# Optimization experiments

Hardware: AMD Instinct MI355X
Metric: run time of the kernel (lower is better)

The kernel has to match this reference:

```python
import jax, jax.numpy as jnp
import numpy as np

EPS = 1e-6
DIM = 2048
N_HEADS = 16
HEAD_DIM = DIM // N_HEADS  # 128
SEQ = 1040
CACHE = 8320
BATCH = 1


def rms_norm(x, g):
    # RMSNorm over the full model dim (WanRMSNorm)
    var = jnp.mean(jnp.square(x.astype(jnp.float32)), axis=-1, keepdims=True)
    return (x.astype(jnp.float32) * jax.lax.rsqrt(var + EPS)).astype(x.dtype) * g


def rope_apply(x, freqs):
    # x: [b, s, n, d]; freqs: [s, d//2] rotation angles (complex rotation on interleaved pairs)
    b, s, n, d = x.shape
    xr = x.reshape(b, s, n, d // 2, 2)
    xe, xo = xr[..., 0], xr[..., 1]
    cos = jnp.cos(freqs)[None, :, None, :]  # [1, s, 1, d//2]
    sin = jnp.sin(freqs)[None, :, None, :]
    out = jnp.stack([xe * cos - xo * sin, xe * sin + xo * cos], axis=-1)
    return out.reshape(b, s, n, d)


def sdpa(q, k, v):
    # q: [b, sq, n, d]; k, v: [b, skv, n, d]
    d = q.shape[-1]
    scale = 1.0 / jnp.sqrt(jnp.asarray(d, dtype=q.dtype))
    scores = jnp.einsum('bqnd,bknd->bnqk', q, k) * scale
    p = jax.nn.softmax(scores, axis=-1)
    return jnp.einsum('bnqk,bknd->bqnd', p, v)


def setup_inputs() -> dict:
    key = jax.random.key(0)
    ks = jax.random.split(key, 16)
    sc = 1.0 / np.sqrt(DIM)
    inp = {
        'x': jax.random.normal(ks[0], (BATCH, SEQ, DIM), dtype=jnp.float32),
        'seq_lens': jnp.full((BATCH,), SEQ, dtype=jnp.int32),
        'freqs': jax.random.uniform(ks[1], (SEQ, HEAD_DIM // 2), dtype=jnp.float32, maxval=2 * np.pi),
        'kv_cache_k': jax.random.normal(ks[2], (BATCH, CACHE, N_HEADS, HEAD_DIM), dtype=jnp.float32),
        'kv_cache_v': jax.random.normal(ks[3], (BATCH, CACHE, N_HEADS, HEAD_DIM), dtype=jnp.float32),
        'Wq': jax.random.normal(ks[4], (DIM, DIM), dtype=jnp.float32) * sc,
        'bq': jnp.zeros((DIM,), dtype=jnp.float32),
        'Wk': jax.random.normal(ks[5], (DIM, DIM), dtype=jnp.float32) * sc,
        'bk': jnp.zeros((DIM,), dtype=jnp.float32),
        'Wv': jax.random.normal(ks[6], (DIM, DIM), dtype=jnp.float32) * sc,
        'bv': jnp.zeros((DIM,), dtype=jnp.float32),
        'Wo': jax.random.normal(ks[7], (DIM, DIM), dtype=jnp.float32) * sc,
        'bo': jnp.zeros((DIM,), dtype=jnp.float32),
        'g_q': jnp.ones((DIM,), dtype=jnp.float32),
        'g_k': jnp.ones((DIM,), dtype=jnp.float32),
        'kv_start': 0,
        'kv_len': CACHE,
    }
    return inp


def reference(x, seq_lens, freqs, kv_cache_k, kv_cache_v, Wq, bq, Wk, bk, Wv, bv, Wo, bo, g_q, g_k, kv_start, kv_len):
    b, s, dim = x.shape
    d = 2 * freqs.shape[-1]
    n = dim // d
    q = rms_norm(x @ Wq + bq, g_q).reshape(b, s, n, d)
    k = rms_norm(x @ Wk + bk, g_k).reshape(b, s, n, d)
    v = (x @ Wv + bv).reshape(b, s, n, d)
    rq = rope_apply(q, freqs)
    rk = rope_apply(k, freqs)
    # kv_size[1] > 0 branch: concat cached KV slice with the new chunk
    k_full = jnp.concatenate([kv_cache_k[:, kv_start:kv_start + kv_len], rk], axis=1)
    v_full = jnp.concatenate([kv_cache_v[:, kv_start:kv_start + kv_len], v], axis=1)
    o = sdpa(rq, k_full, v_full)  # [b, s, n, d]
    return o.reshape(b, s, n * d) @ Wo + bo
```

## Files before the change

### kernel.cpp

```cpp
#include <hip/hip_runtime.h>

using bf16x8 = __attribute__((ext_vector_type(8))) short;
using f32x4  = __attribute__((ext_vector_type(4))) float;

#define DEV static __device__ __forceinline__

constexpr int SEQ    = 1040;
constexpr int MDIM   = 2048;
constexpr int NH     = 16;
constexpr int HD     = 128;
constexpr int NCACHE = 8320;
constexpr int LTOT   = NCACHE + SEQ;
constexpr int KROWS  = 9408;
constexpr int NQT2   = 9;

DEV float b2f(unsigned short u) {
  union { unsigned int i; float f; } z; z.i = ((unsigned int)u) << 16; return z.f;
}
DEV unsigned short f2b(float f) {
  union { float f; unsigned int i; } z; z.f = f;
  return (unsigned short)((z.i + 0x7fffu + ((z.i >> 16) & 1u)) >> 16);
}
DEV unsigned int cvtpk(float lo, float hi) {
  unsigned int r;
  asm("v_cvt_pk_bf16_f32 %0, %1, %2" : "=v"(r) : "v"(lo), "v"(hi));
  return r;
}
union U4S8 { uint4 u; short s[8]; };

__global__ __launch_bounds__(256) void convx_k(
    const float* __restrict__ x, unsigned short* __restrict__ xb, int n8) {
  int i = blockIdx.x * 256 + threadIdx.x;
  if (i < n8) {
    const float* p = x + (size_t)i * 8;
    f32x4 a = *(const f32x4*)p, b = *(const f32x4*)(p + 4);
    uint4 u = make_uint4(cvtpk(a[0], a[1]), cvtpk(a[2], a[3]),
                         cvtpk(b[0], b[1]), cvtpk(b[2], b[3]));
    *(uint4*)(xb + (size_t)i * 8) = u;
  }
}

__global__ __launch_bounds__(256) void convkv_k(
    const float* __restrict__ Kc, const float* __restrict__ Vc,
    unsigned short* __restrict__ Kb, unsigned short* __restrict__ Vb, int n8) {
  int i = blockIdx.x * 256 + threadIdx.x;
  const float* src = blockIdx.y ? Vc : Kc;
  unsigned short* dst = blockIdx.y ? Vb : Kb;
  if (i < n8) {
    const float* p = src + (size_t)i * 8;
    f32x4 a = *(const f32x4*)p, b = *(const f32x4*)(p + 4);
    uint4 u = make_uint4(cvtpk(a[0], a[1]), cvtpk(a[2], a[3]),
                         cvtpk(b[0], b[1]), cvtpk(b[2], b[3]));
    *(uint4*)(dst + (size_t)i * 8) = u;
  }
}

__global__ __launch_bounds__(256) void convt_k(
    const float* __restrict__ W0, const float* __restrict__ W1,
    const float* __restrict__ W2, const float* __restrict__ W3,
    unsigned short* __restrict__ T0, unsigned short* __restrict__ T1,
    unsigned short* __restrict__ T2, unsigned short* __restrict__ T3) {
  __shared__ short T[64][72];
  const int zz = blockIdx.z;
  const float* W = (zz == 0) ? W0 : (zz == 1) ? W1 : (zz == 2) ? W2 : W3;
  unsigned short* O = (zz == 0) ? T0 : (zz == 1) ? T1 : (zz == 2) ? T2 : T3;
  const int r0 = blockIdx.y * 64, c0 = blockIdx.x * 64;
  const int t = threadIdx.x;
  {
    int row = t >> 2, cq = t & 3;
    const float* p = W + (size_t)(r0 + row) * MDIM + c0 + cq * 16;
    f32x4 a = *(const f32x4*)(p);
    f32x4 b = *(const f32x4*)(p + 4);
    f32x4 c = *(const f32x4*)(p + 8);
    f32x4 d = *(const f32x4*)(p + 12);
    *(uint4*)&T[row][cq * 16] =
        make_uint4(cvtpk(a[0], a[1]), cvtpk(a[2], a[3]), cvtpk(b[0], b[1]), cvtpk(b[2], b[3]));
    *(uint4*)&T[row][cq * 16 + 8] =
        make_uint4(cvtpk(c[0], c[1]), cvtpk(c[2], c[3]), cvtpk(d[0], d[1]), cvtpk(d[2], d[3]));
  }
  __syncthreads();
  {
    int c = t >> 2, kq = t & 3;
    U4S8 v0, v1;
#pragma unroll
    for (int i = 0; i < 8; ++i) v0.s[i] = T[kq * 16 + i][c];
#pragma unroll
    for (int i = 0; i < 8; ++i) v1.s[i] = T[kq * 16 + 8 + i][c];
    unsigned short* op = O + (size_t)(c0 + c) * MDIM + r0 + kq * 16;
    *(uint4*)(op) = v0.u;
    *(uint4*)(op + 8) = v1.u;
  }
}

__global__ __launch_bounds__(256) void gemm_qkv_k(
    const unsigned short* __restrict__ xb,
    const unsigned short* __restrict__ Wtq, const unsigned short* __restrict__ Wtk,
    const unsigned short* __restrict__ Wtv,
    const float* __restrict__ bq, const float* __restrict__ bk, const float* __restrict__ bv,
    unsigned short* __restrict__ Qb, unsigned short* __restrict__ Kb, unsigned short* __restrict__ Vb) {
  __shared__ short As[64][72];
  __shared__ short Bs[128][72];
  const int tid = threadIdx.x;
  const int l = tid & 63, wv = tid >> 6;
  const int l16 = l & 15, kl = l >> 4;
  const int m0 = blockIdx.y * 64;
  const int n0g = blockIdx.x * 128;
  const int which = n0g >> 11;
  const int n0 = n0g & 2047;
  const unsigned short* Wt = (which == 0) ? Wtq : (which == 1) ? Wtk : Wtv;
  const float* bias = (which == 0) ? bq : (which == 1) ? bk : bv;
  const int wm = (wv >> 1) * 32, wn = (wv & 1) * 64;
  f32x4 acc[2][4] = {};
  for (int k0 = 0; k0 < MDIM; k0 += 64) {
    {
      int m = tid >> 2, kq = tid & 3;
      int row = m0 + m;
      uint4 v0 = make_uint4(0, 0, 0, 0), v1 = make_uint4(0, 0, 0, 0);
      if (row < SEQ) {
        const unsigned short* p = xb + (size_t)row * MDIM + k0 + kq * 16;
        v0 = *(const uint4*)p;
        v1 = *(const uint4*)(p + 8);
      }
      *(uint4*)&As[m][kq * 16] = v0;
      *(uint4*)&As[m][kq * 16 + 8] = v1;
    }
    {
      int n = tid >> 1, kq = tid & 1;
      const unsigned short* p = Wt + (size_t)(n0 + n) * MDIM + k0 + kq * 32;
      uint4 v0 = *(const uint4*)p, v1 = *(const uint4*)(p + 8);
      uint4 v2 = *(const uint4*)(p + 16), v3 = *(const uint4*)(p + 24);
      *(uint4*)&Bs[n][kq * 32] = v0;
      *(uint4*)&Bs[n][kq * 32 + 8] = v1;
      *(uint4*)&Bs[n][kq * 32 + 16] = v2;
      *(uint4*)&Bs[n][kq * 32 + 24] = v3;
    }
    __syncthreads();
#pragma unroll
    for (int kk = 0; kk < 2; ++kk) {
      bf16x8 aF[2], bF[4];
#pragma unroll
      for (int mi = 0; mi < 2; ++mi)
        aF[mi] = *(const bf16x8*)&As[wm + mi * 16 + l16][kk * 32 + kl * 8];
#pragma unroll
      for (int ni = 0; ni < 4; ++ni)
        bF[ni] = *(const bf16x8*)&Bs[wn + ni * 16 + l16][kk * 32 + kl * 8];
#pragma unroll
      for (int mi = 0; mi < 2; ++mi)
#pragma unroll
        for (int ni = 0; ni < 4; ++ni)
          acc[mi][ni] = __builtin_amdgcn_mfma_f32_16x16x32_bf16(
              aF[mi], bF[ni], acc[mi][ni], 0, 0, 0);
    }
    __syncthreads();
  }
#pragma unroll
  for (int ni = 0; ni < 4; ++ni) {
    const int col = n0 + wn + ni * 16 + l16;
    const float bb = bias[col];
#pragma unroll
    for (int mi = 0; mi < 2; ++mi) {
      const int rowb = m0 + wm + mi * 16 + kl * 4;
#pragma unroll
      for (int r = 0; r < 4; ++r) {
        const int row = rowb + r;
        if (row >= SEQ) continue;
        const unsigned short val = f2b(acc[mi][ni][r] + bb);
        if (which == 0) {
          Qb[((size_t)(col >> 7) * SEQ + row) * HD + (col & 127)] = val;
        } else if (which == 1) {
          Kb[(size_t)(NCACHE + row) * MDIM + col] = val;
        } else {
          Vb[(size_t)(NCACHE + row) * MDIM + col] = val;
        }
      }
    }
  }
}

__global__ __launch_bounds__(256) void gemm_o_k(
    const unsigned short* __restrict__ Ab, const unsigned short* __restrict__ Wt,
    const float* __restrict__ bias, float* __restrict__ outp) {
  __shared__ short As[64][72];
  __shared__ short Bs[128][72];
  const int tid = threadIdx.x;
  const int l = tid & 63, wv = tid >> 6;
  const int l16 = l & 15, kl = l >> 4;
  const int m0 = blockIdx.y * 64, n0 = blockIdx.x * 128;
  const int wm = (wv >> 1) * 32, wn = (wv & 1) * 64;
  f32x4 acc[2][4] = {};
  for (int k0 = 0; k0 < MDIM; k0 += 64) {
    {
      int m = tid >> 2, kq = tid & 3;
      int row = m0 + m, k = k0 + kq * 16;
      uint4 v0 = make_uint4(0, 0, 0, 0), v1 = make_uint4(0, 0, 0, 0);
      if (row < SEQ) {
        const unsigned short* p = Ab + ((size_t)(k >> 7) * SEQ + row) * HD + (k & 127);
        v0 = *(const uint4*)p;
        v1 = *(const uint4*)(p + 8);
      }
      *(uint4*)&As[m][kq * 16] = v0;
      *(uint4*)&As[m][kq * 16 + 8] = v1;
    }
    {
      int n = tid >> 1, kq = tid & 1;
      const unsigned short* p = Wt + (size_t)(n0 + n) * MDIM + k0 + kq * 32;
      uint4 v0 = *(const uint4*)p, v1 = *(const uint4*)(p + 8);
      uint4 v2 = *(const uint4*)(p + 16), v3 = *(const uint4*)(p + 24);
      *(uint4*)&Bs[n][kq * 32] = v0;
      *(uint4*)&Bs[n][kq * 32 + 8] = v1;
      *(uint4*)&Bs[n][kq * 32 + 16] = v2;
      *(uint4*)&Bs[n][kq * 32 + 24] = v3;
    }
    __syncthreads();
#pragma unroll
    for (int kk = 0; kk < 2; ++kk) {
      bf16x8 aF[2], bF[4];
#pragma unroll
      for (int mi = 0; mi < 2; ++mi)
        aF[mi] = *(const bf16x8*)&As[wm + mi * 16 + l16][kk * 32 + kl * 8];
#pragma unroll
      for (int ni = 0; ni < 4; ++ni)
        bF[ni] = *(const bf16x8*)&Bs[wn + ni * 16 + l16][kk * 32 + kl * 8];
#pragma unroll
      for (int mi = 0; mi < 2; ++mi)
#pragma unroll
        for (int ni = 0; ni < 4; ++ni)
          acc[mi][ni] = __builtin_amdgcn_mfma_f32_16x16x32_bf16(
              aF[mi], bF[ni], acc[mi][ni], 0, 0, 0);
    }
    __syncthreads();
  }
#pragma unroll
  for (int ni = 0; ni < 4; ++ni) {
    const int col = n0 + wn + ni * 16 + l16;
    const float bb = bias[col];
#pragma unroll
    for (int mi = 0; mi < 2; ++mi) {
      const int rowb = m0 + wm + mi * 16 + kl * 4;
#pragma unroll
      for (int r = 0; r < 4; ++r) {
        const int row = rowb + r;
        if (row >= SEQ) continue;
        outp[(size_t)row * MDIM + col] = acc[mi][ni][r] + bb;
      }
    }
  }
}

__global__ __launch_bounds__(256) void rmsrope_k(
    unsigned short* __restrict__ Qb, unsigned short* __restrict__ Kb,
    const float* __restrict__ gq, const float* __restrict__ gk,
    const float* __restrict__ fr) {
  const int s = blockIdx.x, which = blockIdx.y;
  const float* g = which ? gk : gq;
  __shared__ float cs[64], sn[64], red[4];
  const int t = threadIdx.x;
  if (t < 64) {
    float a = fr[s * 64 + t];
    cs[t] = cosf(a);
    sn[t] = sinf(a);
  }
  const int c0 = t * 8;
  const int hh = c0 >> 7, dd = c0 & 127, p0 = dd >> 1;
  unsigned short* ptr = which
      ? Kb + (size_t)(NCACHE + s) * MDIM + c0
      : Qb + ((size_t)hh * SEQ + s) * HD + dd;
  bf16x8 v = *(const bf16x8*)ptr;
  float y[8];
#pragma unroll
  for (int i = 0; i < 8; ++i) y[i] = b2f((unsigned short)v[i]);
  float ssq = 0.f;
#pragma unroll
  for (int i = 0; i < 8; ++i) ssq += y[i] * y[i];
#pragma unroll
  for (int off = 32; off; off >>= 1) ssq += __shfl_xor(ssq, off);
  if ((t & 63) == 0) red[t >> 6] = ssq;
  __syncthreads();
  const float var = (red[0] + red[1] + red[2] + red[3]) * (1.0f / MDIM);
  const float rs = rsqrtf(var + 1e-6f);
  bf16x8 ov;
#pragma unroll
  for (int i = 0; i < 4; ++i) {
    float e = b2f(f2b(y[2 * i] * rs)) * g[c0 + 2 * i];
    float o = b2f(f2b(y[2 * i + 1] * rs)) * g[c0 + 2 * i + 1];
    float C = cs[p0 + i], S = sn[p0 + i];
    ov[2 * i]     = (short)f2b(e * C - o * S);
    ov[2 * i + 1] = (short)f2b(e * S + o * C);
  }
  *(bf16x8*)ptr = ov;
}

__global__ __launch_bounds__(512) void attn_part6_k(
    const unsigned short* __restrict__ Qb, const unsigned short* __restrict__ Kb,
    const unsigned short* __restrict__ Vb, unsigned short* __restrict__ Opart,
    float* __restrict__ ml, int chunk, int S) {
  __shared__ short UN[9216];
  __shared__ short Vt[128][72];
  const int b = blockIdx.x;
  const int xcd = b & 7;
  const int r_ = b >> 3;
  const int qt = r_ % NQT2;
  const int g = (r_ / NQT2) * 8 + xcd;
  const int h = g & (NH - 1);
  const int z = g >> 4;
  const int tid = threadIdx.x, wv = tid >> 6, l = tid & 63;
  const int l16 = l & 15, kl = l >> 4;
  const float SCALE = 0.08838834764831845f;

  const int c0 = z * chunk;
  const int cend = min(c0 + chunk, LTOT);

  int qrow = qt * 128 + wv * 16 + l16;
  if (qrow > SEQ - 1) qrow = SEQ - 1;
  bf16x8 qf[4];
#pragma unroll
  for (int kk = 0; kk < 4; ++kk)
    qf[kk] = *(const bf16x8*)(Qb + ((size_t)h * SEQ + qrow) * HD + kk * 32 + kl * 8);

  f32x4 oacc[8] = {};
  float mrow[4] = {-1e30f, -1e30f, -1e30f, -1e30f};
  float lrow[4] = {0.f, 0.f, 0.f, 0.f};

  const int j0 = tid & 63, dq0 = tid >> 6, dq1 = (tid + 512) >> 6;
  const int hofs = h * HD;

  for (int kv0 = c0; kv0 < cend; kv0 += 64) {
    const size_t rbase = (size_t)(kv0 + j0) * MDIM + hofs;
#pragma unroll
    for (int it = 0; it < 2; ++it) {
      const int dq = (it == 0) ? dq0 : dq1;
      uint4 ku = *(const uint4*)(Kb + rbase + dq * 8);
      U4S8 vu; vu.u = *(const uint4*)(Vb + rbase + dq * 8);
      *(uint4*)&UN[j0 * 136 + dq * 8] = ku;
#pragma unroll
      for (int i = 0; i < 8; ++i) Vt[dq * 8 + i][j0] = vu.s[i];
    }
    __syncthreads();

    f32x4 sa[4] = {};
#pragma unroll
    for (int ni = 0; ni < 4; ++ni)
#pragma unroll
      for (int kk = 0; kk < 4; ++kk) {
        bf16x8 bK = *(const bf16x8*)&UN[(ni * 16 + l16) * 136 + kk * 32 + kl * 8];
        sa[ni] = __builtin_amdgcn_mfma_f32_16x16x32_bf16(qf[kk], bK, sa[ni], 0, 0, 0);
      }
    __syncthreads();

    float sv[4][4];
    float pm[4] = {-1e30f, -1e30f, -1e30f, -1e30f};
#pragma unroll
    for (int ni = 0; ni < 4; ++ni) {
      int jg = kv0 + ni * 16 + l16;
      bool valid = jg < LTOT;
#pragma unroll
      for (int r = 0; r < 4; ++r) {
        float xs = valid ? sa[ni][r] * SCALE : -1e30f;
        sv[ni][r] = xs;
        pm[r] = fmaxf(pm[r], xs);
      }
    }
#pragma unroll
    for (int off = 1; off < 16; off <<= 1)
#pragma unroll
      for (int r = 0; r < 4; ++r) pm[r] = fmaxf(pm[r], __shfl_xor(pm[r], off));

    float sc[4];
#pragma unroll
    for (int r = 0; r < 4; ++r) {
      float mn = fmaxf(mrow[r], pm[r]);
      sc[r] = __expf(mrow[r] - mn);
      mrow[r] = mn;
    }
    float ps[4] = {0.f, 0.f, 0.f, 0.f};
#pragma unroll
    for (int ni = 0; ni < 4; ++ni)
#pragma unroll
      for (int r = 0; r < 4; ++r) {
        float p = __expf(sv[ni][r] - mrow[r]);
        sv[ni][r] = p;
        ps[r] += p;
      }
#pragma unroll
    for (int off = 1; off < 16; off <<= 1)
#pragma unroll
      for (int r = 0; r < 4; ++r) ps[r] += __shfl_xor(ps[r], off);
#pragma unroll
    for (int r = 0; r < 4; ++r) lrow[r] = lrow[r] * sc[r] + ps[r];
#pragma unroll
    for (int di = 0; di < 8; ++di)
#pragma unroll
      for (int r = 0; r < 4; ++r) oacc[di][r] *= sc[r];
#pragma unroll
    for (int ni = 0; ni < 4; ++ni)
#pragma unroll
      for (int r = 0; r < 4; ++r)
        UN[(wv * 16 + kl * 4 + r) * 72 + ni * 16 + l16] = (short)f2b(sv[ni][r]);
    __syncthreads();

#pragma unroll
    for (int di = 0; di < 8; ++di)
#pragma unroll
      for (int k2 = 0; k2 < 2; ++k2) {
        bf16x8 aP = *(const bf16x8*)&UN[(wv * 16 + l16) * 72 + k2 * 32 + kl * 8];
        bf16x8 bV = *(const bf16x8*)&Vt[di * 16 + l16][k2 * 32 + kl * 8];
        oacc[di] = __builtin_amdgcn_mfma_f32_16x16x32_bf16(aP, bV, oacc[di], 0, 0, 0);
      }
    __syncthreads();
  }

  const size_t pbase = (((size_t)z * NH + h) * NQT2 + qt);
  const int row = wv * 16 + kl * 4;
#pragma unroll
  for (int r = 0; r < 4; ++r) {
    unsigned short* Op = Opart + (pbase * 128 + row + r) * HD;
#pragma unroll
    for (int di = 0; di < 8; ++di) Op[di * 16 + l16] = f2b(oacc[di][r]);
    ml[(pbase * 2 + 0) * 128 + row + r] = mrow[r];
    ml[(pbase * 2 + 1) * 128 + row + r] = lrow[r];
  }
}

__global__ __launch_bounds__(512) void attn_merge3_k(
    const unsigned short* __restrict__ Opart, const float* __restrict__ ml,
    unsigned short* __restrict__ Qb, int S) {
  const int qt = blockIdx.x, h = blockIdx.y;
  const int t = threadIdx.x;
  const int row = t >> 2, d0 = (t & 3) * 32;
  const int q = qt * 128 + row;

  float M = -1e30f;
  for (int s = 0; s < S; ++s) {
    const size_t pbase = (((size_t)s * NH + h) * NQT2 + qt);
    M = fmaxf(M, ml[(pbase * 2 + 0) * 128 + row]);
  }
  float L = 0.f;
  float o[32];
#pragma unroll
  for (int i = 0; i < 32; ++i) o[i] = 0.f;
  for (int s = 0; s < S; ++s) {
    const size_t pbase = (((size_t)s * NH + h) * NQT2 + qt);
    const float ms = ml[(pbase * 2 + 0) * 128 + row];
    const float ls = ml[(pbase * 2 + 1) * 128 + row];
    const float w = __expf(ms - M);
    L += w * ls;
    const unsigned short* Op = Opart + (pbase * 128 + row) * HD + d0;
#pragma unroll
    for (int c = 0; c < 4; ++c) {
      bf16x8 v = *(const bf16x8*)(Op + c * 8);
#pragma unroll
      for (int i = 0; i < 8; ++i) o[c * 8 + i] += w * b2f((unsigned short)v[i]);
    }
  }
  if (q < SEQ) {
    const float inv = 1.f / L;
    unsigned short* op = Qb + ((size_t)h * SEQ + q) * HD + d0;
#pragma unroll
    for (int i = 0; i < 32; ++i) op[i] = f2b(o[i] * inv);
  }
}

extern "C" void kernel_launch(void* const* d_in, const int* in_sizes, int n_in,
                              void* d_out, int out_size, void* d_ws, size_t ws_size,
                              hipStream_t stream) {
  const float* x  = (const float*)d_in[0];
  const float* fr = (const float*)d_in[2];
  const float* Kc = (const float*)d_in[3];
  const float* Vc = (const float*)d_in[4];
  const float* Wq = (const float*)d_in[5];
  const float* bq = (const float*)d_in[6];
  const float* Wk = (const float*)d_in[7];
  const float* bk = (const float*)d_in[8];
  const float* Wv = (const float*)d_in[9];
  const float* bv = (const float*)d_in[10];
  const float* Wo = (const float*)d_in[11];
  const float* bo = (const float*)d_in[12];
  const float* gq = (const float*)d_in[13];
  const float* gk = (const float*)d_in[14];

  unsigned short* xb  = (unsigned short*)d_ws;
  unsigned short* Wto = xb + (size_t)SEQ * MDIM;
  unsigned short* Qb  = Wto + (size_t)MDIM * MDIM;
  unsigned short* Kb  = Qb + (size_t)NH * SEQ * HD;
  unsigned short* Vb  = Kb + (size_t)KROWS * MDIM;
  unsigned short* Wtq = Vb + (size_t)KROWS * MDIM;
  unsigned short* Wtk = Wtq + (size_t)MDIM * MDIM;
  unsigned short* Wtv = Wtk + (size_t)MDIM * MDIM;
  const size_t fixedB = ((size_t)SEQ * MDIM + (size_t)MDIM * MDIM + (size_t)NH * SEQ * HD
                         + 2 * (size_t)KROWS * MDIM) * 2;
  const size_t aliasB = 3 * (size_t)MDIM * MDIM * 2;

  const size_t perSplitB = (size_t)NH * NQT2 * 128 * HD * 2
                         + (size_t)NH * NQT2 * 2 * 128 * 4;
  int S = 4;
  if (ws_size >= fixedB + aliasB + (8 * perSplitB - aliasB) + (1 << 21)) S = 8;

  unsigned short* Opart = Wtq;
  float* ml = (float*)((char*)Wtq + (size_t)S * NH * NQT2 * 128 * HD * 2);

  const int n8x = SEQ * MDIM / 8;
  const int n8kv = NCACHE * MDIM / 8;
  convx_k<<<dim3((n8x + 255) / 256), 256, 0, stream>>>(x, xb, n8x);
  convkv_k<<<dim3((n8kv + 255) / 256, 2), 256, 0, stream>>>(Kc, Vc, Kb, Vb, n8kv);
  convt_k<<<dim3(32, 32, 4), 256, 0, stream>>>(Wq, Wk, Wv, Wo, Wtq, Wtk, Wtv, Wto);

  gemm_qkv_k<<<dim3(48, 17), 256, 0, stream>>>(xb, Wtq, Wtk, Wtv, bq, bk, bv, Qb, Kb, Vb);
  rmsrope_k<<<dim3(SEQ, 2), 256, 0, stream>>>(Qb, Kb, gq, gk, fr);

  const int tiles = (LTOT + 63) / 64;
  const int chunk = ((tiles + S - 1) / S) * 64;
  attn_part6_k<<<dim3(NQT2 * NH * S), 512, 0, stream>>>(Qb, Kb, Vb, Opart, ml, chunk, S);
  attn_merge3_k<<<dim3(NQT2, NH), 512, 0, stream>>>(Opart, ml, Qb, S);

  gemm_o_k<<<dim3(16, 17), 256, 0, stream>>>(Qb, Wto, bo, (float*)d_out);
}
```

Baseline: 410.4 us.

## Pre-transpose V cache into per-tile head-major layout and fix split count

V is converted into a tiled, transposed bf16 layout (tile, head, dim, 64 keys) during the conversion pass, and the QKV GEMM writes new V rows into the same layout. The attention kernel can then fill its transposed V tile in shared memory with vector stores instead of scalar element scatter. The split count is fixed at 6 instead of being picked from the workspace size (4 or 8), and the last V tile is zeroed with a memset. The conversion now performs the transpose through shared memory, and the new Vbt layout must stay consistent between the producer kernels and the consumer.

```diff
diff --git a/kernel.cpp b/kernel.cpp
--- a/kernel.cpp
+++ b/kernel.cpp
@@ -11,8 +11,10 @@
 constexpr int HD     = 128;
 constexpr int NCACHE = 8320;
 constexpr int LTOT   = NCACHE + SEQ;
-constexpr int KROWS  = 9408;
+constexpr int NTILE  = 147;
+constexpr int KROWS  = NTILE * 64;
 constexpr int NQT2   = 9;
+constexpr int SPLITS = 6;
 
 DEV float b2f(unsigned short u) {
   union { unsigned int i; float f; } z; z.i = ((unsigned int)u) << 16; return z.f;
@@ -40,18 +42,43 @@
   }
 }
 
-__global__ __launch_bounds__(256) void convkv_k(
-    const float* __restrict__ Kc, const float* __restrict__ Vc,
-    unsigned short* __restrict__ Kb, unsigned short* __restrict__ Vb, int n8) {
+__global__ __launch_bounds__(256) void convk_k(
+    const float* __restrict__ Kc, unsigned short* __restrict__ Kb, int n8) {
   int i = blockIdx.x * 256 + threadIdx.x;
-  const float* src = blockIdx.y ? Vc : Kc;
-  unsigned short* dst = blockIdx.y ? Vb : Kb;
   if (i < n8) {
-    const float* p = src + (size_t)i * 8;
+    const float* p = Kc + (size_t)i * 8;
     f32x4 a = *(const f32x4*)p, b = *(const f32x4*)(p + 4);
     uint4 u = make_uint4(cvtpk(a[0], a[1]), cvtpk(a[2], a[3]),
                          cvtpk(b[0], b[1]), cvtpk(b[2], b[3]));
-    *(uint4*)(dst + (size_t)i * 8) = u;
+    *(uint4*)(Kb + (size_t)i * 8) = u;
+  }
+}
+
+__global__ __launch_bounds__(256) void convvt_k(
+    const float* __restrict__ Vc, unsigned short* __restrict__ Vbt) {
+  __shared__ short T[64][136];
+  const int tile = blockIdx.x, h = blockIdx.y;
+  const int t = threadIdx.x;
+  {
+    int row = t >> 2, cq = t & 3;
+    const float* p = Vc + (size_t)(tile * 64 + row) * MDIM + h * HD + cq * 32;
+#pragma unroll
+    for (int k = 0; k < 4; ++k) {
+      f32x4 a = *(const f32x4*)(p + k * 8);
+      f32x4 b = *(const f32x4*)(p + k * 8 + 4);
+      *(uint4*)&T[row][cq * 32 + k * 8] =
+          make_uint4(cvtpk(a[0], a[1]), cvtpk(a[2], a[3]), cvtpk(b[0], b[1]), cvtpk(b[2], b[3]));
+    }
+  }
+  __syncthreads();
+#pragma unroll
+  for (int i = 0; i < 4; ++i) {
+    int c = t + i * 256;
+    int d = c >> 3, joct = c & 7;
+    U4S8 u;
+#pragma unroll
+    for (int jj = 0; jj < 8; ++jj) u.s[jj] = T[joct * 8 + jj][d];
+    *(uint4*)(Vbt + ((((size_t)tile * NH + h) * HD + d) * 64 + joct * 8)) = u.u;
   }
 }
 
@@ -97,7 +124,7 @@
     const unsigned short* __restrict__ Wtq, const unsigned short* __restrict__ Wtk,
     const unsigned short* __restrict__ Wtv,
     const float* __restrict__ bq, const float* __restrict__ bk, const float* __restrict__ bv,
-    unsigned short* __restrict__ Qb, unsigned short* __restrict__ Kb, unsigned short* __restrict__ Vb) {
+    unsigned short* __restrict__ Qb, unsigned short* __restrict__ Kb, unsigned short* __restrict__ Vbt) {
   __shared__ short As[64][72];
   __shared__ short Bs[128][72];
   const int tid = threadIdx.x;
@@ -157,6 +184,7 @@
   for (int ni = 0; ni < 4; ++ni) {
     const int col = n0 + wn + ni * 16 + l16;
     const float bb = bias[col];
+    const int hh = col >> 7, dd = col & 127;
 #pragma unroll
     for (int mi = 0; mi < 2; ++mi) {
       const int rowb = m0 + wm + mi * 16 + kl * 4;
@@ -166,11 +194,12 @@
         if (row >= SEQ) continue;
         const unsigned short val = f2b(acc[mi][ni][r] + bb);
         if (which == 0) {
-          Qb[((size_t)(col >> 7) * SEQ + row) * HD + (col & 127)] = val;
+          Qb[((size_t)hh * SEQ + row) * HD + dd] = val;
         } else if (which == 1) {
           Kb[(size_t)(NCACHE + row) * MDIM + col] = val;
         } else {
-          Vb[(size_t)(NCACHE + row) * MDIM + col] = val;
+          const int g = NCACHE + row;
+          Vbt[(((size_t)(g >> 6) * NH + hh) * HD + dd) * 64 + (g & 63)] = val;
         }
       }
     }
@@ -290,9 +319,9 @@
   *(bf16x8*)ptr = ov;
 }
 
-__global__ __launch_bounds__(512) void attn_part6_k(
+__global__ __launch_bounds__(512) void attn_part7_k(
     const unsigned short* __restrict__ Qb, const unsigned short* __restrict__ Kb,
-    const unsigned short* __restrict__ Vb, unsigned short* __restrict__ Opart,
+    const unsigned short* __restrict__ Vbt, unsigned short* __restrict__ Opart,
     float* __restrict__ ml, int chunk, int S) {
   __shared__ short UN[9216];
   __shared__ short Vt[128][72];
@@ -322,18 +351,21 @@
   float lrow[4] = {0.f, 0.f, 0.f, 0.f};
 
   const int j0 = tid & 63, dq0 = tid >> 6, dq1 = (tid + 512) >> 6;
+  const int dV0 = tid >> 3, dV1 = (tid + 512) >> 3, jo = tid & 7;
   const int hofs = h * HD;
 
   for (int kv0 = c0; kv0 < cend; kv0 += 64) {
-    const size_t rbase = (size_t)(kv0 + j0) * MDIM + hofs;
-#pragma unroll
-    for (int it = 0; it < 2; ++it) {
-      const int dq = (it == 0) ? dq0 : dq1;
-      uint4 ku = *(const uint4*)(Kb + rbase + dq * 8);
-      U4S8 vu; vu.u = *(const uint4*)(Vb + rbase + dq * 8);
-      *(uint4*)&UN[j0 * 136 + dq * 8] = ku;
-#pragma unroll
-      for (int i = 0; i < 8; ++i) Vt[dq * 8 + i][j0] = vu.s[i];
+    {
+      const size_t krow = (size_t)(kv0 + j0) * MDIM + hofs;
+      uint4 k0v = *(const uint4*)(Kb + krow + dq0 * 8);
+      uint4 k1v = *(const uint4*)(Kb + krow + dq1 * 8);
+      const size_t vbase = (((size_t)(kv0 >> 6) * NH + h) * HD) * 64;
+      uint4 v0v = *(const uint4*)(Vbt + vbase + (size_t)dV0 * 64 + jo * 8);
+      uint4 v1v = *(const uint4*)(Vbt + vbase + (size_t)dV1 * 64 + jo * 8);
+      *(uint4*)&UN[j0 * 136 + dq0 * 8] = k0v;
+      *(uint4*)&UN[j0 * 136 + dq1 * 8] = k1v;
+      *(uint4*)&Vt[dV0][jo * 8] = v0v;
+      *(uint4*)&Vt[dV1][jo * 8] = v1v;
     }
     __syncthreads();
 
@@ -482,34 +514,31 @@
   unsigned short* Wto = xb + (size_t)SEQ * MDIM;
   unsigned short* Qb  = Wto + (size_t)MDIM * MDIM;
   unsigned short* Kb  = Qb + (size_t)NH * SEQ * HD;
-  unsigned short* Vb  = Kb + (size_t)KROWS * MDIM;
-  unsigned short* Wtq = Vb + (size_t)KROWS * MDIM;
+  unsigned short* Vbt = Kb + (size_t)KROWS * MDIM;
+  unsigned short* Wtq = Vbt + (size_t)NTILE * NH * HD * 64;
   unsigned short* Wtk = Wtq + (size_t)MDIM * MDIM;
   unsigned short* Wtv = Wtk + (size_t)MDIM * MDIM;
-  const size_t fixedB = ((size_t)SEQ * MDIM + (size_t)MDIM * MDIM + (size_t)NH * SEQ * HD
-                         + 2 * (size_t)KROWS * MDIM) * 2;
-  const size_t aliasB = 3 * (size_t)MDIM * MDIM * 2;
-
-  const size_t perSplitB = (size_t)NH * NQT2 * 128 * HD * 2
-                         + (size_t)NH * NQT2 * 2 * 128 * 4;
-  int S = 4;
-  if (ws_size >= fixedB + aliasB + (8 * perSplitB - aliasB) + (1 << 21)) S = 8;
-
+
+  const int S = SPLITS;
   unsigned short* Opart = Wtq;
-  float* ml = (float*)((char*)Wtq + (size_t)S * NH * NQT2 * 128 * HD * 2);
+  float* ml = (float*)(Opart + (size_t)S * NH * NQT2 * 128 * HD);
+
+  hipMemsetAsync(Vbt + (size_t)(NTILE - 1) * NH * HD * 64, 0,
+                 (size_t)NH * HD * 64 * 2, stream);
 
   const int n8x = SEQ * MDIM / 8;
-  const int n8kv = NCACHE * MDIM / 8;
+  const int n8k = NCACHE * MDIM / 8;
   convx_k<<<dim3((n8x + 255) / 256), 256, 0, stream>>>(x, xb, n8x);
-  convkv_k<<<dim3((n8kv + 255) / 256, 2), 256, 0, stream>>>(Kc, Vc, Kb, Vb, n8kv);
+  convk_k<<<dim3((n8k + 255) / 256), 256, 0, stream>>>(Kc, Kb, n8k);
+  convvt_k<<<dim3(NCACHE / 64, NH), 256, 0, stream>>>(Vc, Vbt);
   convt_k<<<dim3(32, 32, 4), 256, 0, stream>>>(Wq, Wk, Wv, Wo, Wtq, Wtk, Wtv, Wto);
 
-  gemm_qkv_k<<<dim3(48, 17), 256, 0, stream>>>(xb, Wtq, Wtk, Wtv, bq, bk, bv, Qb, Kb, Vb);
+  gemm_qkv_k<<<dim3(48, 17), 256, 0, stream>>>(xb, Wtq, Wtk, Wtv, bq, bk, bv, Qb, Kb, Vbt);
   rmsrope_k<<<dim3(SEQ, 2), 256, 0, stream>>>(Qb, Kb, gq, gk, fr);
 
-  const int tiles = (LTOT + 63) / 64;
+  const int tiles = NTILE;
   const int chunk = ((tiles + S - 1) / S) * 64;
-  attn_part6_k<<<dim3(NQT2 * NH * S), 512, 0, stream>>>(Qb, Kb, Vb, Opart, ml, chunk, S);
+  attn_part7_k<<<dim3(NQT2 * NH * S), 512, 0, stream>>>(Qb, Kb, Vbt, Opart, ml, chunk, S);
   attn_merge3_k<<<dim3(NQT2, NH), 512, 0, stream>>>(Opart, ml, Qb, S);
 
   gemm_o_k<<<dim3(16, 17), 256, 0, stream>>>(Qb, Wto, bo, (float*)d_out);
```

Measured after the change: 405.4 us. About the same (-1.2%).
